# Performance work log

Measured on AMD Instinct MI355X. Metric: run time of the kernel, lower is better.

The kernel has to match this reference:

```python
import jax, jax.numpy as jnp
import numpy as np

K = 3       # kernel size
PAD = 1
IMG = 512   # hard-coded img_size in source
CIN = 32
COUT = 32
B = 1
NORI = 8    # output_stabilizer_size


def make_group_mask(size=IMG, n=NORI):
    # group_conv_8mask: partition image into 8 angular sectors around the
    # fisheye center -> one-hot [8, H, W] mask selecting one orientation per pixel.
    c = (size - 1) / 2.0
    yy, xx = np.meshgrid(np.arange(size), np.arange(size), indexing='ij')
    ang = np.arctan2(yy - c, xx - c)  # [-pi, pi]
    sector = (np.floor((ang + np.pi) / (2.0 * np.pi) * n).astype(np.int64)) % n
    m = np.zeros((n, size, size), np.float32)
    m[sector.reshape(-1), yy.reshape(-1), xx.reshape(-1)] = 1.0
    return m


def rotate_kernel(w, deg):
    # bilinear rotation of [..., K, K] kernel about its center, zero fill (TorchRotate)
    th = np.deg2rad(deg)
    c = (K - 1) / 2.0
    ii, jj = jnp.meshgrid(jnp.arange(K, dtype=jnp.float32), jnp.arange(K, dtype=jnp.float32), indexing='ij')
    cos, sin = np.cos(th).astype(np.float32), np.sin(th).astype(np.float32)
    ys = cos * (ii - c) + sin * (jj - c) + c   # inverse-rotated source coords
    xs = -sin * (ii - c) + cos * (jj - c) + c
    y0 = jnp.floor(ys); x0 = jnp.floor(xs)
    wy = ys - y0; wx = xs - x0
    out = jnp.zeros_like(w)
    for dy, wy_ in ((0, 1.0 - wy), (1, wy)):
        for dx, wx_ in ((0, 1.0 - wx), (1, wx)):
            iy = (y0 + dy).astype(jnp.int32); ix = (x0 + dx).astype(jnp.int32)
            valid = ((iy >= 0) & (iy < K) & (ix >= 0) & (ix < K)).astype(w.dtype)
            iyc = jnp.clip(iy, 0, K - 1); ixc = jnp.clip(ix, 0, K - 1)
            out = out + w[..., iyc, ixc] * (wy_ * wx_ * valid)
    return out


def conv2d(x, w, b):
    y = jax.lax.conv_general_dilated(x, w, (1, 1), ((PAD, PAD), (PAD, PAD)),
                                     dimension_numbers=('NCHW', 'OIHW', 'NCHW'))
    return y + b[None, :, None, None]


def bilinear_gather(x, py, px):
    # x: [Cin, H, W]; py/px: [KK, H, W] fractional sample coords (zero outside)
    H, W = x.shape[-2], x.shape[-1]
    y0 = jnp.floor(py); x0 = jnp.floor(px)
    wy = py - y0; wx = px - x0
    out = jnp.zeros((x.shape[0],) + py.shape, x.dtype)
    for dy, wy_ in ((0, 1.0 - wy), (1, wy)):
        for dx, wx_ in ((0, 1.0 - wx), (1, wx)):
            iy = (y0 + dy).astype(jnp.int32); ix = (x0 + dx).astype(jnp.int32)
            valid = ((iy >= 0) & (iy < H) & (ix >= 0) & (ix < W)).astype(x.dtype)
            iyc = jnp.clip(iy, 0, H - 1); ixc = jnp.clip(ix, 0, W - 1)
            g = x[:, iyc, ixc]  # [Cin, KK, H, W]
            out = out + g * (wy_ * wx_ * valid)[None]
    return out


def _forward(x, weight, offset_w, offset_b, mask_w, mask_b, group_mask):
    # --- group-equivariant weight transform: 8 orientations (0/90/180/270 + 45-rotated set)
    base = weight[:, :, 0]                                        # [Cout, Cin, K, K]
    rots = [jnp.rot90(base, k=r, axes=(-2, -1)) for r in range(4)]
    w45 = rotate_kernel(base, 45.0)
    rots45 = [jnp.rot90(w45, k=r, axes=(-2, -1)) for r in range(4)]
    tw = jnp.stack(rots + rots45, axis=1)                         # [Cout, 8, Cin, K, K]
    tw = tw.reshape(COUT * NORI, CIN, K * K)

    H, W = x.shape[-2], x.shape[-1]
    offset = conv2d(x, offset_w, offset_b)                        # [B, 2*KK, H, W]
    modm = conv2d(x, mask_w, mask_b)                              # [B, KK, H, W]
    offset = offset.at[:, 8:10].set(0.0)                          # center-tap offsets zeroed
    modm = jax.nn.sigmoid(modm.at[:, 4].set(0.0))                 # center-tap logit zeroed

    off = offset.reshape(B, K * K, 2, H, W)                       # (dy, dx) pairs per tap
    ky, kx = jnp.meshgrid(jnp.arange(K, dtype=x.dtype), jnp.arange(K, dtype=x.dtype), indexing='ij')
    py = jnp.arange(H, dtype=x.dtype)[None, :, None] - PAD + ky.reshape(-1, 1, 1)
    px = jnp.arange(W, dtype=x.dtype)[None, None, :] - PAD + kx.reshape(-1, 1, 1)
    py = py[None] + off[:, :, 0]                                  # [B, KK, H, W]
    px = px[None] + off[:, :, 1]

    sampled = jax.vmap(bilinear_gather)(x, py, px)                # [B, Cin, KK, H, W]
    sampled = sampled * modm[:, None]                             # modulation
    y = jnp.einsum('bckhw,ock->bohw', sampled, tw)                # [B, Cout*8, H, W]
    y = y.reshape(B, COUT, NORI, H, W)
    y = jax.nn.relu(y)
    y = y * group_mask[None, None]                                # adaptive pool is identity at stride 1
    return y.sum(axis=2)                                          # [B, Cout, H, W]


def setup_inputs() -> dict:
    key = jax.random.key(0)
    ks = jax.random.split(key, 6)
    stdv = float(1.0 / np.sqrt(CIN * K * K))
    return {
        'input': jax.random.normal(ks[0], (B, CIN, IMG, IMG), jnp.float32),
        'weight': jax.random.uniform(ks[1], (COUT, CIN, 1, K, K), jnp.float32, -stdv, stdv),
        'offset_w': jax.random.normal(ks[2], (2 * K * K, CIN, K, K), jnp.float32) * 0.01,
        'offset_b': jax.random.normal(ks[3], (2 * K * K,), jnp.float32) * 0.01,
        'mask_w': jax.random.normal(ks[4], (K * K, CIN, K, K), jnp.float32) * 0.01,
        'mask_b': jax.random.normal(ks[5], (K * K,), jnp.float32) * 0.01,
        'group_mask': jnp.asarray(make_group_mask()),
    }


def reference(input, weight, offset_w, offset_b, mask_w, mask_b, group_mask):
    return _forward(input, weight, offset_w, offset_b, mask_w, mask_b, group_mask)
```

## Files before the change

### kernel.cpp

```cpp
#include <hip/hip_runtime.h>

#define IMG 512
#define CIN 32
#define COUT 32
#define NORI 8
#define HW (IMG*IMG)

#define TS 16

#define W1 18
#define WR1 19
#define CHS1P 346
#define HALO 4
#define WIN 24
#define WROW 25
#define CHSP 602

typedef _Float16 h2 __attribute__((ext_vector_type(2)));
typedef __fp16  fp16v2 __attribute__((ext_vector_type(2)));
typedef _Float16 f16x8 __attribute__((ext_vector_type(8)));
typedef float    f32x4 __attribute__((ext_vector_type(4)));

__device__ __forceinline__ float dot2acc(unsigned int a, unsigned int b, float c) {
#if __has_builtin(__builtin_amdgcn_fdot2)
    return __builtin_amdgcn_fdot2(__builtin_bit_cast(h2, a),
                                  __builtin_bit_cast(h2, b), c, false);
#else
    h2 av = __builtin_bit_cast(h2, a), bv = __builtin_bit_cast(h2, b);
    return fmaf((float)av[0], (float)bv[0], fmaf((float)av[1], (float)bv[1], c));
#endif
}

__device__ __forceinline__ unsigned int packh2(float a, float b) {
#if __has_builtin(__builtin_amdgcn_cvt_pkrtz)
    fp16v2 r = __builtin_amdgcn_cvt_pkrtz(a, b);
    return __builtin_bit_cast(unsigned int, r);
#else
    h2 r; r[0] = (_Float16)a; r[1] = (_Float16)b;
    return __builtin_bit_cast(unsigned int, r);
#endif
}

__device__ __forceinline__ unsigned int packh2_rne(float a, float b) {
    h2 r; r[0] = (_Float16)a; r[1] = (_Float16)b;
    return __builtin_bit_cast(unsigned int, r);
}

#define GEMV8(TP, S2) do {                                             \
    const uint4* _tp = (TP);                                           \
    _Pragma("unroll")                                                  \
    for (int q = 0; q < 8; ++q) {                                      \
        uint4 u = _tp[q];                                              \
        oacc[q * 4 + 0] = dot2acc((S2), u.x, oacc[q * 4 + 0]);         \
        oacc[q * 4 + 1] = dot2acc((S2), u.y, oacc[q * 4 + 1]);         \
        oacc[q * 4 + 2] = dot2acc((S2), u.z, oacc[q * 4 + 2]);         \
        oacc[q * 4 + 3] = dot2acc((S2), u.w, oacc[q * 4 + 3]);         \
    }                                                                  \
} while (0)

__global__ void build_tw_kernel(const float* __restrict__ weight, unsigned int* __restrict__ tw_h) {
    int idx = blockIdx.x * blockDim.x + threadIdx.x;
    if (idx >= COUT * (CIN / 2)) return;
    int o = idx & 31, cp = idx >> 5;

    float bb[2][9], w45[2][9];
    const float cs = 0.70710678f;
#pragma unroll
    for (int h = 0; h < 2; ++h) {
        int c = 2 * cp + h;
#pragma unroll
        for (int t = 0; t < 9; ++t) bb[h][t] = weight[(o * CIN + c) * 9 + t];
#pragma unroll
        for (int i = 0; i < 3; ++i) {
#pragma unroll
            for (int j = 0; j < 3; ++j) {
                float ys = cs * (float)(i - 1) + cs * (float)(j - 1) + 1.0f;
                float xs = -cs * (float)(i - 1) + cs * (float)(j - 1) + 1.0f;
                float y0f = floorf(ys), x0f = floorf(xs);
                float wy = ys - y0f, wx = xs - x0f;
                int iy0 = (int)y0f, ix0 = (int)x0f;
                float a = 0.0f;
#pragma unroll
                for (int dy = 0; dy < 2; ++dy) {
#pragma unroll
                    for (int dx = 0; dx < 2; ++dx) {
                        int iy = iy0 + dy, ix = ix0 + dx;
                        float wgt = (dy ? wy : 1.0f - wy) * (dx ? wx : 1.0f - wx);
                        bool valid = (iy >= 0) && (iy < 3) && (ix >= 0) && (ix < 3);
                        int iyc = min(max(iy, 0), 2), ixc = min(max(ix, 0), 2);
                        a += bb[h][iyc * 3 + ixc] * (valid ? wgt : 0.0f);
                    }
                }
                w45[h][i * 3 + j] = a;
            }
        }
    }

#pragma unroll
    for (int r = 0; r < NORI; ++r) {
        int rr = r & 3;
#pragma unroll
        for (int i = 0; i < 3; ++i) {
#pragma unroll
            for (int j = 0; j < 3; ++j) {
                int si, sj;
                if (rr == 0) { si = i;     sj = j;     }
                else if (rr == 1) { si = j;     sj = 2 - i; }
                else if (rr == 2) { si = 2 - i; sj = 2 - j; }
                else { si = 2 - j; sj = i;     }
                float v0 = (r < 4) ? bb[0][si * 3 + sj] : w45[0][si * 3 + sj];
                float v1 = (r < 4) ? bb[1][si * 3 + sj] : w45[1][si * 3 + sj];
                tw_h[(((r * 9) + (i * 3 + j)) * (CIN / 2) + cp) * COUT + o] =
                    packh2_rne(v0, v1);
            }
        }
    }
}

__global__ void pack_owmb_kernel(const float* __restrict__ offw, const float* __restrict__ mskw,
                                 unsigned int* __restrict__ owmb) {
    int idx = blockIdx.x * blockDim.x + threadIdx.x;
    if (idx >= 9 * 16 * 32) return;
    int oc = idx & 31;
    int cp = (idx >> 5) & 15;
    int kt = idx >> 9;
    float v0 = 0.0f, v1 = 0.0f;
    if (oc < 18) {
        v0 = offw[(oc * CIN + 2 * cp) * 9 + kt];
        v1 = offw[(oc * CIN + 2 * cp + 1) * 9 + kt];
    } else if (oc < 27) {
        v0 = mskw[((oc - 18) * CIN + 2 * cp) * 9 + kt];
        v1 = mskw[((oc - 18) * CIN + 2 * cp + 1) * 9 + kt];
    }
    owmb[(kt * 16 + cp) * 32 + oc] = packh2_rne(v0, v1);
}

__global__ __launch_bounds__(256, 4) void offset_mask_mfma_kernel(
    const float* __restrict__ x,
    const unsigned int* __restrict__ owmb,
    const float* __restrict__ offb, const float* __restrict__ mskb,
    float* __restrict__ om)
{
    __shared__ unsigned int Lp[16 * CHS1P];

    const int tiles_x = IMG / TS;
    int bid = (int)blockIdx.x;
    bid = (bid % 8) * (1024 / 8) + bid / 8;
    int bx = bid % tiles_x, by = bid / tiles_x;
    int tid = threadIdx.x;
    int y0w = by * TS - 1, x0w = bx * TS - 1;

    for (int i = tid; i < 16 * (W1 * W1); i += 256) {
        int pr = i / (W1 * W1), cell = i % (W1 * W1);
        int rr = cell / W1, cc = cell % W1;
        int gy = y0w + rr, gx = x0w + cc;
        float a = 0.0f, b = 0.0f;
        if ((unsigned)gy < (unsigned)IMG && (unsigned)gx < (unsigned)IMG) {
            const float* x0 = x + (2 * pr) * HW + gy * IMG + gx;
            a = x0[0]; b = x0[HW];
        }
        Lp[pr * CHS1P + rr * WR1 + cc] = packh2_rne(a, b);
    }
    __syncthreads();

    int lane = tid & 63, wid = tid >> 6;
    int lrow = lane & 15, lhi = lane >> 4;

    f32x4 acc[4][2] = {};

#pragma unroll
    for (int kt = 0; kt < 9; ++kt) {
        const int ky = kt / 3, kx = kt % 3;
        const unsigned int* tb = owmb + (kt * 16 + lhi * 4) * 32 + lrow;
        unsigned int bu0[4], bu1[4];
#pragma unroll
        for (int jj = 0; jj < 4; ++jj) {
            bu0[jj] = tb[jj * 32];
            bu1[jj] = tb[jj * 32 + 16];
        }
        uint4 b0q = make_uint4(bu0[0], bu0[1], bu0[2], bu0[3]);
        uint4 b1q = make_uint4(bu1[0], bu1[1], bu1[2], bu1[3]);
        f16x8 bf0 = __builtin_bit_cast(f16x8, b0q);
        f16x8 bf1 = __builtin_bit_cast(f16x8, b1q);

#pragma unroll
        for (int mt = 0; mt < 4; ++mt) {
            int yy = wid * 4 + mt;
            int lq = (yy + ky) * WR1 + (lrow + kx);
            unsigned int au[4];
#pragma unroll
            for (int j = 0; j < 4; ++j)
                au[j] = Lp[(lhi * 4 + j) * CHS1P + lq];
            uint4 aq = make_uint4(au[0], au[1], au[2], au[3]);
            f16x8 af = __builtin_bit_cast(f16x8, aq);
            acc[mt][0] = __builtin_amdgcn_mfma_f32_16x16x32_f16(af, bf0, acc[mt][0], 0, 0, 0);
            acc[mt][1] = __builtin_amdgcn_mfma_f32_16x16x32_f16(af, bf1, acc[mt][1], 0, 0, 0);
        }
    }

    float bias_n0 = offb[lrow];
    float bias_n1 = (lrow < 2) ? offb[16 + lrow]
                  : ((lrow < 11) ? mskb[lrow - 2] : 0.0f);
    int Xs = bx * 16 + lhi * 4;
#pragma unroll
    for (int mt = 0; mt < 4; ++mt) {
        int Yg = by * 16 + wid * 4 + mt;
        {
            int oc = lrow;
            float* op = om + oc * HW + Yg * IMG + Xs;
            bool zero = (oc == 8) || (oc == 9);
#pragma unroll
            for (int q = 0; q < 4; ++q)
                op[q] = zero ? 0.0f : (acc[mt][0][q] + bias_n0);
        }
        {
            int oc = 16 + lrow;
            if (oc < 27) {
                float* op = om + oc * HW + Yg * IMG + Xs;
#pragma unroll
                for (int q = 0; q < 4; ++q) {
                    float t = acc[mt][1][q] + bias_n1;
                    if (oc >= 18) t = (oc == 22) ? 0.5f : 1.0f / (1.0f + __expf(-t));
                    op[q] = t;
                }
            }
        }
    }
}

__global__ __launch_bounds__(256, 3) void deform_mfma_kernel(
    const float* __restrict__ x,
    const float* __restrict__ om,
    const float* __restrict__ gm,
    const unsigned int* __restrict__ tw_h,
    float* __restrict__ out)
{
    __shared__ unsigned int Lx[16 * CHSP];
    __shared__ uint2 Wl[3 * 256];
    __shared__ unsigned short LQ[3 * 256];
    __shared__ int flags[2];

    const int tiles_x = IMG / TS;
    int bid = (int)blockIdx.x;
    bid = (bid % 8) * (1024 / 8) + bid / 8;
    int bx = bid % tiles_x, by = bid / tiles_x;
    int tid = threadIdx.x;
    int tx = tid & 15, ty = tid >> 4;
    int X = bx * TS + tx, Y = by * TS + ty;
    int p = Y * IMG + X;
    int y0w = by * TS - HALO, x0w = bx * TS - HALO;

    if (tid < 2) flags[tid] = 0;
    __syncthreads();

    for (int i = tid; i < 16 * (WIN * WIN); i += 256) {
        int pr = i / (WIN * WIN), cell = i % (WIN * WIN);
        int rr = cell / WIN, cc = cell % WIN;
        int gy = y0w + rr, gx = x0w + cc;
        float a = 0.0f, b = 0.0f;
        if ((unsigned)gy < (unsigned)IMG && (unsigned)gx < (unsigned)IMG) {
            const float* x0 = x + (2 * pr) * HW + gy * IMG + gx;
            a = x0[0]; b = x0[HW];
        }
        Lx[pr * CHSP + rr * WROW + cc] = packh2_rne(a, b);
    }

    int r = 0;
#pragma unroll
    for (int n = 1; n < NORI; ++n) r = (gm[n * HW + p] > 0.5f) ? n : r;

    bool slow = false;
    for (int kt = 0; kt < 9; ++kt) {
        int ky = kt / 3, kx = kt - ky * 3;
        float offy = om[(2 * kt) * HW + p];
        float offx = om[(2 * kt + 1) * HW + p];
        float pyf = (float)(Y - 1 + ky) + offy;
        float pxf = (float)(X - 1 + kx) + offx;
        int iy0 = (int)floorf(pyf), ix0 = (int)floorf(pxf);
        int ryu = iy0 - y0w, rxu = ix0 - x0w;
        slow |= !(((unsigned)ryu < (WIN - 1)) && ((unsigned)rxu < (WIN - 1)));
    }
    atomicOr(&flags[0], 1 << r);
    if (slow) flags[1] = 1;
    __syncthreads();

    int rmaskv = __builtin_amdgcn_readfirstlane(flags[0]);
    int anyslow = flags[1];

    if (anyslow) {
        float oacc[32];
#pragma unroll
        for (int o = 0; o < 32; ++o) oacc[o] = 0.0f;
        for (int kt = 0; kt < 9; ++kt) {
            int ky = kt / 3, kx = kt - ky * 3;
            float offy = om[(2 * kt) * HW + p];
            float offx = om[(2 * kt + 1) * HW + p];
            float m    = om[(18 + kt) * HW + p];
            float pyf = (float)(Y - 1 + ky) + offy;
            float pxf = (float)(X - 1 + kx) + offx;
            float y0f = floorf(pyf), x0f = floorf(pxf);
            float wy = pyf - y0f, wx = pxf - x0f;
            int iy0 = (int)y0f, ix0 = (int)x0f;
            float vy0 = ((unsigned)iy0 < (unsigned)IMG) ? 1.0f : 0.0f;
            float vy1 = ((unsigned)(iy0 + 1) < (unsigned)IMG) ? 1.0f : 0.0f;
            float vx0 = ((unsigned)ix0 < (unsigned)IMG) ? 1.0f : 0.0f;
            float vx1 = ((unsigned)(ix0 + 1) < (unsigned)IMG) ? 1.0f : 0.0f;
            float w00 = m * (1.0f - wy) * (1.0f - wx) * vy0 * vx0;
            float w01 = m * (1.0f - wy) * wx * vy0 * vx1;
            float w10 = m * wy * (1.0f - wx) * vy1 * vx0;
            float w11 = m * wy * wx * vy1 * vx1;
            int cy0 = min(max(iy0, 0), IMG - 1), cy1 = min(max(iy0 + 1, 0), IMG - 1);
            int cx0 = min(max(ix0, 0), IMG - 1), cx1 = min(max(ix0 + 1, 0), IMG - 1);
            int g00 = cy0 * IMG + cx0, g01 = cy0 * IMG + cx1;
            int g10 = cy1 * IMG + cx0, g11 = cy1 * IMG + cx1;
            const uint4* tp = (const uint4*)(tw_h + (unsigned)((r * 9 + kt) * (CIN / 2)) * COUT);
            for (int cp = 0; cp < CIN / 2; ++cp) {
                const float* xc0 = x + (2 * cp) * HW;
                const float* xc1 = xc0 + HW;
                float s0 = fmaf(w00, xc0[g00], fmaf(w01, xc0[g01],
                           fmaf(w10, xc0[g10], w11 * xc0[g11])));
                float s1 = fmaf(w00, xc1[g00], fmaf(w01, xc1[g01],
                           fmaf(w10, xc1[g10], w11 * xc1[g11])));
                unsigned int s2 = packh2(s0, s1);
                GEMV8(tp + cp * 8, s2);
            }
        }
#pragma unroll
        for (int o = 0; o < 32; ++o) out[o * HW + p] = fmaxf(oacc[o], 0.0f);
        return;
    }

    int lane = tid & 63, wid = tid >> 6;
    int lrow = lane & 15, lhi = lane >> 4;

    f32x4 acc[4][2] = {};

    for (int g = 0; g < 3; ++g) {
#pragma unroll
        for (int kt2 = 0; kt2 < 3; ++kt2) {
            int kt = g * 3 + kt2;
            int ky = kt / 3, kx = kt - ky * 3;
            float offy = om[(2 * kt) * HW + p];
            float offx = om[(2 * kt + 1) * HW + p];
            float m    = om[(18 + kt) * HW + p];
            float pyf = (float)(Y - 1 + ky) + offy;
            float pxf = (float)(X - 1 + kx) + offx;
            float y0f = floorf(pyf), x0f = floorf(pxf);
            float wy = pyf - y0f, wx = pxf - x0f;
            int iy0 = (int)y0f, ix0 = (int)x0f;
            float vy0 = ((unsigned)iy0 < (unsigned)IMG) ? 1.0f : 0.0f;
            float vy1 = ((unsigned)(iy0 + 1) < (unsigned)IMG) ? 1.0f : 0.0f;
            float vx0 = ((unsigned)ix0 < (unsigned)IMG) ? 1.0f : 0.0f;
            float vx1 = ((unsigned)(ix0 + 1) < (unsigned)IMG) ? 1.0f : 0.0f;
            float w00 = m * (1.0f - wy) * (1.0f - wx) * vy0 * vx0;
            float w01 = m * (1.0f - wy) * wx * vy0 * vx1;
            float w10 = m * wy * (1.0f - wx) * vy1 * vx0;
            float w11 = m * wy * wx * vy1 * vx1;
            int lq = (iy0 - y0w) * WROW + (ix0 - x0w);
            Wl[kt2 * 256 + tid] = make_uint2(packh2_rne(w00, w01), packh2_rne(w10, w11));
            LQ[kt2 * 256 + tid] = (unsigned short)(lq | (r << 12));
        }
        __syncthreads();

        int rm = rmaskv;
        while (rm) {
            int rr = __ffs(rm) - 1;
            rm &= rm - 1;
#pragma unroll
            for (int kt2 = 0; kt2 < 3; ++kt2) {
                int kt = g * 3 + kt2;
                const unsigned int* tb = tw_h +
                    (unsigned)((rr * 9 + kt) * (CIN / 2) + lhi * 4) * COUT + lrow;
                unsigned int bu0[4], bu1[4];
#pragma unroll
                for (int jj = 0; jj < 4; ++jj) {
                    bu0[jj] = tb[jj * COUT];
                    bu1[jj] = tb[jj * COUT + 16];
                }
                uint4 b0q = make_uint4(bu0[0], bu0[1], bu0[2], bu0[3]);
                uint4 b1q = make_uint4(bu1[0], bu1[1], bu1[2], bu1[3]);
                f16x8 bf0 = __builtin_bit_cast(f16x8, b0q);
                f16x8 bf1 = __builtin_bit_cast(f16x8, b1q);

#pragma unroll
                for (int mt = 0; mt < 4; ++mt) {
                    int px = (wid * 4 + mt) * 16 + lrow;
                    uint2 wv = Wl[kt2 * 256 + px];
                    int lqr = (int)LQ[kt2 * 256 + px];
                    int lq = lqr & 0xFFF;
                    unsigned int keep = ((lqr >> 12) == rr) ? 0xFFFFFFFFu : 0u;
                    h2 wpa = __builtin_bit_cast(h2, wv.x);
                    h2 wpb = __builtin_bit_cast(h2, wv.y);
                    h2 w00h = __builtin_shufflevector(wpa, wpa, 0, 0);
                    h2 w01h = __builtin_shufflevector(wpa, wpa, 1, 1);
                    h2 w10h = __builtin_shufflevector(wpb, wpb, 0, 0);
                    h2 w11h = __builtin_shufflevector(wpb, wpb, 1, 1);
                    unsigned int au[4];
#pragma unroll
                    for (int j = 0; j < 4; ++j) {
                        int lb = (lhi * 4 + j) * CHSP + lq;
                        h2 v00 = __builtin_bit_cast(h2, Lx[lb]);
                        h2 v01 = __builtin_bit_cast(h2, Lx[lb + 1]);
                        h2 v10 = __builtin_bit_cast(h2, Lx[lb + WROW]);
                        h2 v11 = __builtin_bit_cast(h2, Lx[lb + WROW + 1]);
                        h2 s = w00h * v00 + w01h * v01 + w10h * v10 + w11h * v11;
                        au[j] = __builtin_bit_cast(unsigned int, s) & keep;
                    }
                    uint4 aq = make_uint4(au[0], au[1], au[2], au[3]);
                    f16x8 af = __builtin_bit_cast(f16x8, aq);
                    acc[mt][0] = __builtin_amdgcn_mfma_f32_16x16x32_f16(af, bf0, acc[mt][0], 0, 0, 0);
                    acc[mt][1] = __builtin_amdgcn_mfma_f32_16x16x32_f16(af, bf1, acc[mt][1], 0, 0, 0);
                }
            }
        }
        __syncthreads();
    }

    int Xs = bx * 16 + lhi * 4;
#pragma unroll
    for (int mt = 0; mt < 4; ++mt) {
        int Yg = by * 16 + wid * 4 + mt;
#pragma unroll
        for (int nt = 0; nt < 2; ++nt) {
            float* op = out + (nt * 16 + lrow) * HW + Yg * IMG + Xs;
#pragma unroll
            for (int q = 0; q < 4; ++q)
                op[q] = fmaxf(acc[mt][nt][q], 0.0f);
        }
    }
}

extern "C" void kernel_launch(void* const* d_in, const int* in_sizes, int n_in,
                              void* d_out, int out_size, void* d_ws, size_t ws_size,
                              hipStream_t stream) {
    const float* x      = (const float*)d_in[0];
    const float* weight = (const float*)d_in[1];
    const float* offw   = (const float*)d_in[2];
    const float* offb   = (const float*)d_in[3];
    const float* mskw   = (const float*)d_in[4];
    const float* mskb   = (const float*)d_in[5];
    const float* gm     = (const float*)d_in[6];
    float* out = (float*)d_out;

    unsigned int* tw_h = (unsigned int*)d_ws;
    unsigned int* owmb = (unsigned int*)((char*)d_ws + 147456);
    float* om = (float*)((char*)d_ws + 294912);

    build_tw_kernel<<<2, 256, 0, stream>>>(weight, tw_h);
    pack_owmb_kernel<<<18, 256, 0, stream>>>(offw, mskw, owmb);

    const int tiles = (IMG / TS) * (IMG / TS);
    offset_mask_mfma_kernel<<<tiles, 256, 0, stream>>>(x, owmb, offb, mskb, om);
    deform_mfma_kernel<<<tiles, 256, 0, stream>>>(x, om, gm, tw_h, out);
}
```

Before: 95.62 us.

## Compute bilinear weights per lane in MFMA layout, dropping LDS staging and barriers

Each lane now loads the offsets and mask and computes the bilinear weights and window index for the four pixels it feeds into the MFMA A operand. This replaces the per-thread computation that was staged through shared memory (Wl/LQ) and read back after a __syncthreads. It removes the per-group barriers and LDS round trips. Only the orientation index is still kept in LDS. Launch bounds are raised to 4 blocks per SIMD, which adds register pressure, and the om loads are now repeated by the four lhi lane groups (4x redundant global reads and weight math).

```diff
diff --git a/kernel.cpp b/kernel.cpp
--- a/kernel.cpp
+++ b/kernel.cpp
@@ -44,6 +44,12 @@
 __device__ __forceinline__ unsigned int packh2_rne(float a, float b) {
     h2 r; r[0] = (_Float16)a; r[1] = (_Float16)b;
     return __builtin_bit_cast(unsigned int, r);
+}
+
+__device__ __forceinline__ h2 splat2(float a) {
+    _Float16 h = (_Float16)a;
+    h2 r; r[0] = h; r[1] = h;
+    return r;
 }
 
 #define GEMV8(TP, S2) do {                                             \
@@ -228,7 +234,7 @@
     }
 }
 
-__global__ __launch_bounds__(256, 3) void deform_mfma_kernel(
+__global__ __launch_bounds__(256, 4) void deform_mfma_kernel(
     const float* __restrict__ x,
     const float* __restrict__ om,
     const float* __restrict__ gm,
@@ -236,8 +242,7 @@
     float* __restrict__ out)
 {
     __shared__ unsigned int Lx[16 * CHSP];
-    __shared__ uint2 Wl[3 * 256];
-    __shared__ unsigned short LQ[3 * 256];
+    __shared__ unsigned short Rr[256];
     __shared__ int flags[2];
 
     const int tiles_x = IMG / TS;
@@ -268,6 +273,7 @@
     int r = 0;
 #pragma unroll
     for (int n = 1; n < NORI; ++n) r = (gm[n * HW + p] > 0.5f) ? n : r;
+    Rr[tid] = (unsigned short)r;
 
     bool slow = false;
     for (int kt = 0; kt < 9; ++kt) {
@@ -332,19 +338,24 @@
 
     int lane = tid & 63, wid = tid >> 6;
     int lrow = lane & 15, lhi = lane >> 4;
+    int Xg = bx * 16 + lrow;
 
     f32x4 acc[4][2] = {};
 
-    for (int g = 0; g < 3; ++g) {
-#pragma unroll
-        for (int kt2 = 0; kt2 < 3; ++kt2) {
-            int kt = g * 3 + kt2;
-            int ky = kt / 3, kx = kt - ky * 3;
-            float offy = om[(2 * kt) * HW + p];
-            float offx = om[(2 * kt + 1) * HW + p];
-            float m    = om[(18 + kt) * HW + p];
-            float pyf = (float)(Y - 1 + ky) + offy;
-            float pxf = (float)(X - 1 + kx) + offx;
+    for (int kt = 0; kt < 9; ++kt) {
+        int ky = kt / 3, kx = kt - ky * 3;
+        h2 W00[4], W01[4], W10[4], W11[4];
+        int LQv[4], Rv[4];
+#pragma unroll
+        for (int mt = 0; mt < 4; ++mt) {
+            int pyg = by * 16 + wid * 4 + mt;
+            int pg = pyg * IMG + Xg;
+            int px = (wid * 4 + mt) * 16 + lrow;
+            float offy = om[(2 * kt) * HW + pg];
+            float offx = om[(2 * kt + 1) * HW + pg];
+            float m    = om[(18 + kt) * HW + pg];
+            float pyf = (float)(pyg - 1 + ky) + offy;
+            float pxf = (float)(Xg - 1 + kx) + offx;
             float y0f = floorf(pyf), x0f = floorf(pxf);
             float wy = pyf - y0f, wx = pxf - x0f;
             int iy0 = (int)y0f, ix0 = (int)x0f;
@@ -352,68 +363,52 @@
             float vy1 = ((unsigned)(iy0 + 1) < (unsigned)IMG) ? 1.0f : 0.0f;
             float vx0 = ((unsigned)ix0 < (unsigned)IMG) ? 1.0f : 0.0f;
             float vx1 = ((unsigned)(ix0 + 1) < (unsigned)IMG) ? 1.0f : 0.0f;
-            float w00 = m * (1.0f - wy) * (1.0f - wx) * vy0 * vx0;
-            float w01 = m * (1.0f - wy) * wx * vy0 * vx1;
-            float w10 = m * wy * (1.0f - wx) * vy1 * vx0;
-            float w11 = m * wy * wx * vy1 * vx1;
-            int lq = (iy0 - y0w) * WROW + (ix0 - x0w);
-            Wl[kt2 * 256 + tid] = make_uint2(packh2_rne(w00, w01), packh2_rne(w10, w11));
-            LQ[kt2 * 256 + tid] = (unsigned short)(lq | (r << 12));
-        }
-        __syncthreads();
+            W00[mt] = splat2(m * (1.0f - wy) * (1.0f - wx) * vy0 * vx0);
+            W01[mt] = splat2(m * (1.0f - wy) * wx * vy0 * vx1);
+            W10[mt] = splat2(m * wy * (1.0f - wx) * vy1 * vx0);
+            W11[mt] = splat2(m * wy * wx * vy1 * vx1);
+            LQv[mt] = (iy0 - y0w) * WROW + (ix0 - x0w);
+            Rv[mt]  = (int)Rr[px];
+        }
 
         int rm = rmaskv;
         while (rm) {
             int rr = __ffs(rm) - 1;
             rm &= rm - 1;
-#pragma unroll
-            for (int kt2 = 0; kt2 < 3; ++kt2) {
-                int kt = g * 3 + kt2;
-                const unsigned int* tb = tw_h +
-                    (unsigned)((rr * 9 + kt) * (CIN / 2) + lhi * 4) * COUT + lrow;
-                unsigned int bu0[4], bu1[4];
-#pragma unroll
-                for (int jj = 0; jj < 4; ++jj) {
-                    bu0[jj] = tb[jj * COUT];
-                    bu1[jj] = tb[jj * COUT + 16];
+            const unsigned int* tb = tw_h +
+                (unsigned)((rr * 9 + kt) * (CIN / 2) + lhi * 4) * COUT + lrow;
+            unsigned int bu0[4], bu1[4];
+#pragma unroll
+            for (int jj = 0; jj < 4; ++jj) {
+                bu0[jj] = tb[jj * COUT];
+                bu1[jj] = tb[jj * COUT + 16];
+            }
+            uint4 b0q = make_uint4(bu0[0], bu0[1], bu0[2], bu0[3]);
+            uint4 b1q = make_uint4(bu1[0], bu1[1], bu1[2], bu1[3]);
+            f16x8 bf0 = __builtin_bit_cast(f16x8, b0q);
+            f16x8 bf1 = __builtin_bit_cast(f16x8, b1q);
+
+#pragma unroll
+            for (int mt = 0; mt < 4; ++mt) {
+                unsigned int keep = (Rv[mt] == rr) ? 0xFFFFFFFFu : 0u;
+                int lq = LQv[mt];
+                unsigned int au[4];
+#pragma unroll
+                for (int j = 0; j < 4; ++j) {
+                    int lb = (lhi * 4 + j) * CHSP + lq;
+                    h2 v00 = __builtin_bit_cast(h2, Lx[lb]);
+                    h2 v01 = __builtin_bit_cast(h2, Lx[lb + 1]);
+                    h2 v10 = __builtin_bit_cast(h2, Lx[lb + WROW]);
+                    h2 v11 = __builtin_bit_cast(h2, Lx[lb + WROW + 1]);
+                    h2 s = W00[mt] * v00 + W01[mt] * v01 + W10[mt] * v10 + W11[mt] * v11;
+                    au[j] = __builtin_bit_cast(unsigned int, s) & keep;
                 }
-                uint4 b0q = make_uint4(bu0[0], bu0[1], bu0[2], bu0[3]);
-                uint4 b1q = make_uint4(bu1[0], bu1[1], bu1[2], bu1[3]);
-                f16x8 bf0 = __builtin_bit_cast(f16x8, b0q);
-                f16x8 bf1 = __builtin_bit_cast(f16x8, b1q);
-
-#pragma unroll
-                for (int mt = 0; mt < 4; ++mt) {
-                    int px = (wid * 4 + mt) * 16 + lrow;
-                    uint2 wv = Wl[kt2 * 256 + px];
-                    int lqr = (int)LQ[kt2 * 256 + px];
-                    int lq = lqr & 0xFFF;
-                    unsigned int keep = ((lqr >> 12) == rr) ? 0xFFFFFFFFu : 0u;
-                    h2 wpa = __builtin_bit_cast(h2, wv.x);
-                    h2 wpb = __builtin_bit_cast(h2, wv.y);
-                    h2 w00h = __builtin_shufflevector(wpa, wpa, 0, 0);
-                    h2 w01h = __builtin_shufflevector(wpa, wpa, 1, 1);
-                    h2 w10h = __builtin_shufflevector(wpb, wpb, 0, 0);
-                    h2 w11h = __builtin_shufflevector(wpb, wpb, 1, 1);
-                    unsigned int au[4];
-#pragma unroll
-                    for (int j = 0; j < 4; ++j) {
-                        int lb = (lhi * 4 + j) * CHSP + lq;
-                        h2 v00 = __builtin_bit_cast(h2, Lx[lb]);
-                        h2 v01 = __builtin_bit_cast(h2, Lx[lb + 1]);
-                        h2 v10 = __builtin_bit_cast(h2, Lx[lb + WROW]);
-                        h2 v11 = __builtin_bit_cast(h2, Lx[lb + WROW + 1]);
-                        h2 s = w00h * v00 + w01h * v01 + w10h * v10 + w11h * v11;
-                        au[j] = __builtin_bit_cast(unsigned int, s) & keep;
-                    }
-                    uint4 aq = make_uint4(au[0], au[1], au[2], au[3]);
-                    f16x8 af = __builtin_bit_cast(f16x8, aq);
-                    acc[mt][0] = __builtin_amdgcn_mfma_f32_16x16x32_f16(af, bf0, acc[mt][0], 0, 0, 0);
-                    acc[mt][1] = __builtin_amdgcn_mfma_f32_16x16x32_f16(af, bf1, acc[mt][1], 0, 0, 0);
-                }
-            }
-        }
-        __syncthreads();
+                uint4 aq = make_uint4(au[0], au[1], au[2], au[3]);
+                f16x8 af = __builtin_bit_cast(f16x8, aq);
+                acc[mt][0] = __builtin_amdgcn_mfma_f32_16x16x32_f16(af, bf0, acc[mt][0], 0, 0, 0);
+                acc[mt][1] = __builtin_amdgcn_mfma_f32_16x16x32_f16(af, bf1, acc[mt][1], 0, 0, 0);
+            }
+        }
     }
 
     int Xs = bx * 16 + lhi * 4;
```

Result: faster. 85.60 us (-10.5%).

## Process one kernel tap per barrier, hoist bilinear weights, tighten LDS stride for occupancy

Applied to the files above, without the earlier changes.

Restructures the deformable sampling loop from groups of three taps per barrier to one tap per barrier. The per-pixel bilinear weights and sample indices are now read from shared memory into registers once per tap, not once per orientation iteration. The LDS window row stride drops from 25 to 24 and the Wl/LQ staging buffers shrink, cutting shared memory so launch bounds can rise from 3 to 4 blocks per CU. The cost is three times as many __syncthreads calls. The unpadded row stride may also cause more LDS bank conflicts, and holding the hoisted weights adds register pressure.

```diff
diff --git a/kernel.cpp b/kernel.cpp
--- a/kernel.cpp
+++ b/kernel.cpp
@@ -13,8 +13,8 @@
 #define CHS1P 346
 #define HALO 4
 #define WIN 24
-#define WROW 25
-#define CHSP 602
+#define WROW 24
+#define CHSP 578
 
 typedef _Float16 h2 __attribute__((ext_vector_type(2)));
 typedef __fp16  fp16v2 __attribute__((ext_vector_type(2)));
@@ -228,7 +228,7 @@
     }
 }
 
-__global__ __launch_bounds__(256, 3) void deform_mfma_kernel(
+__global__ __launch_bounds__(256, 4) void deform_mfma_kernel(
     const float* __restrict__ x,
     const float* __restrict__ om,
     const float* __restrict__ gm,
@@ -236,8 +236,8 @@
     float* __restrict__ out)
 {
     __shared__ unsigned int Lx[16 * CHSP];
-    __shared__ uint2 Wl[3 * 256];
-    __shared__ unsigned short LQ[3 * 256];
+    __shared__ uint2 Wl[256];
+    __shared__ unsigned int LQa[256];
     __shared__ int flags[2];
 
     const int tiles_x = IMG / TS;
@@ -335,11 +335,9 @@
 
     f32x4 acc[4][2] = {};
 
-    for (int g = 0; g < 3; ++g) {
-#pragma unroll
-        for (int kt2 = 0; kt2 < 3; ++kt2) {
-            int kt = g * 3 + kt2;
-            int ky = kt / 3, kx = kt - ky * 3;
+    for (int kt = 0; kt < 9; ++kt) {
+        int ky = kt / 3, kx = kt - ky * 3;
+        {
             float offy = om[(2 * kt) * HW + p];
             float offx = om[(2 * kt + 1) * HW + p];
             float m    = om[(18 + kt) * HW + p];
@@ -356,61 +354,64 @@
             float w01 = m * (1.0f - wy) * wx * vy0 * vx1;
             float w10 = m * wy * (1.0f - wx) * vy1 * vx0;
             float w11 = m * wy * wx * vy1 * vx1;
-            int lq = (iy0 - y0w) * WROW + (ix0 - x0w);
-            Wl[kt2 * 256 + tid] = make_uint2(packh2_rne(w00, w01), packh2_rne(w10, w11));
-            LQ[kt2 * 256 + tid] = (unsigned short)(lq | (r << 12));
+            Wl[tid]  = make_uint2(packh2_rne(w00, w01), packh2_rne(w10, w11));
+            LQa[tid] = (unsigned)((iy0 - y0w) * WROW + (ix0 - x0w)) | ((unsigned)r << 12);
         }
         __syncthreads();
+
+        h2 W00[4], W01[4], W10[4], W11[4];
+        int LQv[4], Rv[4];
+#pragma unroll
+        for (int mt = 0; mt < 4; ++mt) {
+            int px = (wid * 4 + mt) * 16 + lrow;
+            uint2 wv = Wl[px];
+            unsigned lqr = LQa[px];
+            h2 wpa = __builtin_bit_cast(h2, wv.x);
+            h2 wpb = __builtin_bit_cast(h2, wv.y);
+            W00[mt] = __builtin_shufflevector(wpa, wpa, 0, 0);
+            W01[mt] = __builtin_shufflevector(wpa, wpa, 1, 1);
+            W10[mt] = __builtin_shufflevector(wpb, wpb, 0, 0);
+            W11[mt] = __builtin_shufflevector(wpb, wpb, 1, 1);
+            LQv[mt] = (int)(lqr & 0xFFF);
+            Rv[mt]  = (int)(lqr >> 12);
+        }
 
         int rm = rmaskv;
         while (rm) {
             int rr = __ffs(rm) - 1;
             rm &= rm - 1;
-#pragma unroll
-            for (int kt2 = 0; kt2 < 3; ++kt2) {
-                int kt = g * 3 + kt2;
-                const unsigned int* tb = tw_h +
-                    (unsigned)((rr * 9 + kt) * (CIN / 2) + lhi * 4) * COUT + lrow;
-                unsigned int bu0[4], bu1[4];
-#pragma unroll
-                for (int jj = 0; jj < 4; ++jj) {
-                    bu0[jj] = tb[jj * COUT];
-                    bu1[jj] = tb[jj * COUT + 16];
+            const unsigned int* tb = tw_h +
+                (unsigned)((rr * 9 + kt) * (CIN / 2) + lhi * 4) * COUT + lrow;
+            unsigned int bu0[4], bu1[4];
+#pragma unroll
+            for (int jj = 0; jj < 4; ++jj) {
+                bu0[jj] = tb[jj * COUT];
+                bu1[jj] = tb[jj * COUT + 16];
+            }
+            uint4 b0q = make_uint4(bu0[0], bu0[1], bu0[2], bu0[3]);
+            uint4 b1q = make_uint4(bu1[0], bu1[1], bu1[2], bu1[3]);
+            f16x8 bf0 = __builtin_bit_cast(f16x8, b0q);
+            f16x8 bf1 = __builtin_bit_cast(f16x8, b1q);
+
+#pragma unroll
+            for (int mt = 0; mt < 4; ++mt) {
+                unsigned int keep = (Rv[mt] == rr) ? 0xFFFFFFFFu : 0u;
+                int lq = LQv[mt];
+                unsigned int au[4];
+#pragma unroll
+                for (int j = 0; j < 4; ++j) {
+                    int lb = (lhi * 4 + j) * CHSP + lq;
+                    h2 v00 = __builtin_bit_cast(h2, Lx[lb]);
+                    h2 v01 = __builtin_bit_cast(h2, Lx[lb + 1]);
+                    h2 v10 = __builtin_bit_cast(h2, Lx[lb + WROW]);
+                    h2 v11 = __builtin_bit_cast(h2, Lx[lb + WROW + 1]);
+                    h2 s = W00[mt] * v00 + W01[mt] * v01 + W10[mt] * v10 + W11[mt] * v11;
+                    au[j] = __builtin_bit_cast(unsigned int, s) & keep;
                 }
-                uint4 b0q = make_uint4(bu0[0], bu0[1], bu0[2], bu0[3]);
-                uint4 b1q = make_uint4(bu1[0], bu1[1], bu1[2], bu1[3]);
-                f16x8 bf0 = __builtin_bit_cast(f16x8, b0q);
-                f16x8 bf1 = __builtin_bit_cast(f16x8, b1q);
-
-#pragma unroll
-                for (int mt = 0; mt < 4; ++mt) {
-                    int px = (wid * 4 + mt) * 16 + lrow;
-                    uint2 wv = Wl[kt2 * 256 + px];
-                    int lqr = (int)LQ[kt2 * 256 + px];
-                    int lq = lqr & 0xFFF;
-                    unsigned int keep = ((lqr >> 12) == rr) ? 0xFFFFFFFFu : 0u;
-                    h2 wpa = __builtin_bit_cast(h2, wv.x);
-                    h2 wpb = __builtin_bit_cast(h2, wv.y);
-                    h2 w00h = __builtin_shufflevector(wpa, wpa, 0, 0);
-                    h2 w01h = __builtin_shufflevector(wpa, wpa, 1, 1);
-                    h2 w10h = __builtin_shufflevector(wpb, wpb, 0, 0);
-                    h2 w11h = __builtin_shufflevector(wpb, wpb, 1, 1);
-                    unsigned int au[4];
-#pragma unroll
-                    for (int j = 0; j < 4; ++j) {
-                        int lb = (lhi * 4 + j) * CHSP + lq;
-                        h2 v00 = __builtin_bit_cast(h2, Lx[lb]);
-                        h2 v01 = __builtin_bit_cast(h2, Lx[lb + 1]);
-                        h2 v10 = __builtin_bit_cast(h2, Lx[lb + WROW]);
-                        h2 v11 = __builtin_bit_cast(h2, Lx[lb + WROW + 1]);
-                        h2 s = w00h * v00 + w01h * v01 + w10h * v10 + w11h * v11;
-                        au[j] = __builtin_bit_cast(unsigned int, s) & keep;
-                    }
-                    uint4 aq = make_uint4(au[0], au[1], au[2], au[3]);
-                    f16x8 af = __builtin_bit_cast(f16x8, aq);
-                    acc[mt][0] = __builtin_amdgcn_mfma_f32_16x16x32_f16(af, bf0, acc[mt][0], 0, 0, 0);
-                    acc[mt][1] = __builtin_amdgcn_mfma_f32_16x16x32_f16(af, bf1, acc[mt][1], 0, 0, 0);
-                }
+                uint4 aq = make_uint4(au[0], au[1], au[2], au[3]);
+                f16x8 af = __builtin_bit_cast(f16x8, aq);
+                acc[mt][0] = __builtin_amdgcn_mfma_f32_16x16x32_f16(af, bf0, acc[mt][0], 0, 0, 0);
+                acc[mt][1] = __builtin_amdgcn_mfma_f32_16x16x32_f16(af, bf1, acc[mt][1], 0, 0, 0);
             }
         }
         __syncthreads();
```

After: 84.24 us. 11.9% less time.
